# Performance work log

Hardware: AMD Instinct MI355X
Metric: run time of the kernel (lower is better)

Reference implementation:

```python
import jax, jax.numpy as jnp
import numpy as np

B, H, W, DM = 32, 32, 32, 128   # batch, height, width, d_model
DIN, N, R = 64, 16, 8           # d_inner(low_dim), d_state, dt_rank=ceil(128/16)
LN_EPS = 1e-5


def setup_inputs() -> dict:
    key = jax.random.key(0)
    ks = jax.random.split(key, 10)
    x = jax.random.normal(ks[0], (B, H, W, DM), dtype=jnp.float32)
    w_in = jax.random.normal(ks[1], (2 * DIN, DM), dtype=jnp.float32) * 0.02
    conv_w = jax.random.normal(ks[2], (DIN, 1, 3, 3), dtype=jnp.float32) * 0.1
    conv_b = jax.random.normal(ks[3], (DIN,), dtype=jnp.float32) * 0.01
    xproj_w = jax.random.normal(ks[4], (R + 2 * N, DIN), dtype=jnp.float32) * 0.05
    dtproj_w = jax.random.uniform(ks[5], (DIN, R), dtype=jnp.float32,
                                  minval=-(R ** -0.5), maxval=R ** -0.5)
    # dt bias init: inverse-softplus of dt ~ LogUniform(1e-3, 0.1)
    dt = jnp.exp(jax.random.uniform(ks[6], (DIN,)) * (np.log(0.1) - np.log(0.001)) + np.log(0.001))
    dt = jnp.clip(dt, 1e-4, None)
    dtproj_b = dt + jnp.log(-jnp.expm1(-dt))
    A_logs = jnp.log(jnp.broadcast_to(jnp.arange(1, N + 1, dtype=jnp.float32), (DIN, N)))
    Ds = jnp.ones((DIN,), dtype=jnp.float32)
    ln_g = jnp.ones((DIN,), dtype=jnp.float32)
    ln_b = jnp.zeros((DIN,), dtype=jnp.float32)
    w_out = jax.random.normal(ks[7], (DM, DIN), dtype=jnp.float32) * 0.02
    return {"x": x, "w_in": w_in, "conv_w": conv_w, "conv_b": conv_b,
            "xproj_w": xproj_w, "dtproj_w": dtproj_w, "dtproj_b": dtproj_b,
            "A_logs": A_logs, "Ds": Ds, "ln_g": ln_g, "ln_b": ln_b, "w_out": w_out}


def _silu(v):
    return v * jax.nn.sigmoid(v)


def reference(x, w_in, conv_w, conv_b, xproj_w, dtproj_w, dtproj_b,
              A_logs, Ds, ln_g, ln_b, w_out):
    b, h, w, _ = x.shape
    L = h * w
    # in_proj (no bias) and gate split
    xz = jnp.einsum('bhwc,ec->bhwe', x, w_in)           # [B,H,W,2*DIN]
    xc, z = jnp.split(xz, 2, axis=-1)
    # depthwise conv2d, SAME padding (k=3, pad=1), then SiLU
    xc = jnp.transpose(xc, (0, 3, 1, 2))                # [B,DIN,H,W]
    xc = jax.lax.conv_general_dilated(
        xc, conv_w, window_strides=(1, 1), padding=((1, 1), (1, 1)),
        feature_group_count=DIN, dimension_numbers=('NCHW', 'OIHW', 'NCHW'))
    xc = _silu(xc + conv_b[None, :, None, None])
    u = xc.reshape(b, DIN, L)                            # [B,D,L]
    # x_proj -> dt, B, C
    x_dbl = jnp.einsum('bdl,cd->bcl', u, xproj_w)        # [B,R+2N,L]
    dts, Bs, Cs = x_dbl[:, :R], x_dbl[:, R:R + N], x_dbl[:, R + N:]
    delta = jnp.einsum('brl,dr->bdl', dts, dtproj_w) + dtproj_b[None, :, None]
    delta = jax.nn.softplus(delta)                       # [B,D,L]
    A = -jnp.exp(A_logs)                                 # [D,N]
    dA = jnp.exp(delta[..., None] * A[None, :, None, :])               # [B,D,L,N]
    dBu = (delta * u)[..., None] * jnp.swapaxes(Bs, 1, 2)[:, None]     # [B,D,L,N]
    # sequential selective scan over L
    dA_s = jnp.moveaxis(dA, 2, 0)                        # [L,B,D,N]
    dBu_s = jnp.moveaxis(dBu, 2, 0)
    C_s = jnp.moveaxis(Cs, 2, 0)                         # [L,B,N]

    def step(hst, inp):
        dA_t, dBu_t, C_t = inp
        hst = dA_t * hst + dBu_t                         # [B,D,N]
        y_t = jnp.einsum('bdn,bn->bd', hst, C_t)
        return hst, y_t

    h0 = jnp.zeros((b, DIN, N), dtype=u.dtype)
    _, ys = jax.lax.scan(step, h0, (dA_s, dBu_s, C_s))   # ys: [L,B,D]
    y = jnp.moveaxis(ys, 0, 2) + Ds[None, :, None] * u   # [B,D,L]
    # back to [B,H,W,D], layernorm, gate, out_proj
    y = jnp.swapaxes(y, 1, 2).reshape(b, h, w, DIN)
    mu = jnp.mean(y, axis=-1, keepdims=True)
    var = jnp.var(y, axis=-1, keepdims=True)
    y = (y - mu) * jax.lax.rsqrt(var + LN_EPS) * ln_g + ln_b
    y = y * _silu(z)
    return jnp.einsum('bhwd,cd->bhwc', y, w_out)
```

## Files before the change

kernel.cpp:

```cpp
#include <hip/hip_runtime.h>


__global__ __launch_bounds__(256) void k1_gemm_in(
    const float* __restrict__ x, const float* __restrict__ w_in,
    float* __restrict__ xc, float* __restrict__ z)
{
    __shared__ float As[32 * 68];
    __shared__ float Ws[32 * 132];
    const int t  = threadIdx.x;
    const int p0 = blockIdx.x * 64;
    const int tx = t & 15, ty = t >> 4;

    float acc[4][8];
#pragma unroll
    for (int i = 0; i < 4; ++i)
#pragma unroll
        for (int j = 0; j < 8; ++j) acc[i][j] = 0.f;

    for (int kk = 0; kk < 128; kk += 32) {
        {
            const int m  = t >> 3;
            const int c4 = (t & 7) * 4;
            const float4 v0 = *reinterpret_cast<const float4*>(&x[(size_t)(p0 + m) * 128 + kk + c4]);
            const float4 v1 = *reinterpret_cast<const float4*>(&x[(size_t)(p0 + m + 32) * 128 + kk + c4]);
            As[(c4 + 0) * 68 + m] = v0.x; As[(c4 + 1) * 68 + m] = v0.y;
            As[(c4 + 2) * 68 + m] = v0.z; As[(c4 + 3) * 68 + m] = v0.w;
            As[(c4 + 0) * 68 + m + 32] = v1.x; As[(c4 + 1) * 68 + m + 32] = v1.y;
            As[(c4 + 2) * 68 + m + 32] = v1.z; As[(c4 + 3) * 68 + m + 32] = v1.w;
        }
        for (int i = t; i < 4096; i += 256) {
            const int c = i & 31, e = i >> 5;
            Ws[c * 132 + e] = w_in[(size_t)e * 128 + kk + c];
        }
        __syncthreads();
#pragma unroll
        for (int k = 0; k < 32; ++k) {
            const float4 a  = *reinterpret_cast<const float4*>(&As[k * 68 + (ty << 2)]);
            const float4 b0 = *reinterpret_cast<const float4*>(&Ws[k * 132 + (tx << 3)]);
            const float4 b1 = *reinterpret_cast<const float4*>(&Ws[k * 132 + (tx << 3) + 4]);
            const float am[4] = {a.x, a.y, a.z, a.w};
            const float bm[8] = {b0.x, b0.y, b0.z, b0.w, b1.x, b1.y, b1.z, b1.w};
#pragma unroll
            for (int i = 0; i < 4; ++i)
#pragma unroll
                for (int j = 0; j < 8; ++j)
                    acc[i][j] = fmaf(am[i], bm[j], acc[i][j]);
        }
        __syncthreads();
    }

    const int b  = p0 >> 10;
    const int l0 = (p0 & 1023) + (ty << 2);
    if (tx < 8) {
#pragma unroll
        for (int j = 0; j < 8; ++j) {
            const int e = (tx << 3) + j;
            *reinterpret_cast<float4*>(&xc[((size_t)b * 64 + e) * 1024 + l0]) =
                make_float4(acc[0][j], acc[1][j], acc[2][j], acc[3][j]);
        }
    } else {
        const int d0 = (tx - 8) << 3;
#pragma unroll
        for (int i = 0; i < 4; ++i) {
            const size_t p = (size_t)p0 + (ty << 2) + i;
            *reinterpret_cast<float4*>(&z[p * 64 + d0]) =
                make_float4(acc[i][0], acc[i][1], acc[i][2], acc[i][3]);
            *reinterpret_cast<float4*>(&z[p * 64 + d0 + 4]) =
                make_float4(acc[i][4], acc[i][5], acc[i][6], acc[i][7]);
        }
    }
}

__global__ __launch_bounds__(256) void k2_conv(
    const float* __restrict__ xc, const float* __restrict__ cw,
    const float* __restrict__ cb, float* __restrict__ u)
{
    __shared__ float pl[1024];
    const int bd = blockIdx.x;
    const int t  = threadIdx.x;
    const int d  = bd & 63;
    reinterpret_cast<float4*>(pl)[t] =
        reinterpret_cast<const float4*>(xc + (size_t)bd * 1024)[t];
    float w[9];
#pragma unroll
    for (int i = 0; i < 9; ++i) w[i] = cw[d * 9 + i];
    const float bias = cb[d];
    __syncthreads();
    float o[4];
#pragma unroll
    for (int i = 0; i < 4; ++i) {
        const int p  = t * 4 + i;
        const int py = p >> 5, px = p & 31;
        float s = 0.f;
#pragma unroll
        for (int ky = 0; ky < 3; ++ky) {
            const int iy = py + ky - 1;
            if (iy < 0 || iy > 31) continue;
#pragma unroll
            for (int kx = 0; kx < 3; ++kx) {
                const int ix = px + kx - 1;
                if (ix < 0 || ix > 31) continue;
                s = fmaf(pl[iy * 32 + ix], w[ky * 3 + kx], s);
            }
        }
        s += bias;
        o[i] = s / (1.f + __expf(-s));
    }
    reinterpret_cast<float4*>(u + (size_t)bd * 1024)[t] = make_float4(o[0], o[1], o[2], o[3]);
}

__global__ __launch_bounds__(256) void k3_xproj(
    const float* __restrict__ u, const float* __restrict__ xpw,
    const float* __restrict__ dtw_g, const float* __restrict__ dtb,
    float* __restrict__ delta, float* __restrict__ Bsp, float* __restrict__ Csp)
{
    __shared__ float ut[64][33];
    __shared__ float xd[40][33];
    __shared__ float xw[64 * 40];
    __shared__ float dwv[512];
    const int t   = threadIdx.x;
    const int blk = blockIdx.x;
    const int b   = blk >> 5;
    const int l0  = (blk & 31) * 32;

    for (int i = t; i < 2560; i += 256) {
        const int dd = i / 40, c = i - dd * 40;
        xw[i] = xpw[(size_t)c * 64 + dd];
    }
    for (int i = t; i < 512; i += 256) dwv[i] = dtw_g[i];

    {
        const int dd = t >> 2;
        const int lq = (t & 3) * 8;
        const float* up = u + ((size_t)b * 64 + dd) * 1024 + l0 + lq;
        const float4 v0 = *reinterpret_cast<const float4*>(up);
        const float4 v1 = *reinterpret_cast<const float4*>(up + 4);
        ut[dd][lq + 0] = v0.x; ut[dd][lq + 1] = v0.y;
        ut[dd][lq + 2] = v0.z; ut[dd][lq + 3] = v0.w;
        ut[dd][lq + 4] = v1.x; ut[dd][lq + 5] = v1.y;
        ut[dd][lq + 6] = v1.z; ut[dd][lq + 7] = v1.w;
    }
    __syncthreads();

    {
        const int pix = t & 31, cg = t >> 5;
        const int c0 = cg * 5;
        float a0 = 0.f, a1 = 0.f, a2 = 0.f, a3 = 0.f, a4 = 0.f;
#pragma unroll 8
        for (int dd = 0; dd < 64; ++dd) {
            const float uv = ut[dd][pix];
            const float* row = &xw[dd * 40 + c0];
            a0 = fmaf(uv, row[0], a0);
            a1 = fmaf(uv, row[1], a1);
            a2 = fmaf(uv, row[2], a2);
            a3 = fmaf(uv, row[3], a3);
            a4 = fmaf(uv, row[4], a4);
        }
        xd[c0 + 0][pix] = a0; xd[c0 + 1][pix] = a1; xd[c0 + 2][pix] = a2;
        xd[c0 + 3][pix] = a3; xd[c0 + 4][pix] = a4;
    }
    __syncthreads();

    {
        const int pix = t & 31, nn = t >> 5;
        float* bp = Bsp + (size_t)b * 16384 + l0 + pix;
        float* cp = Csp + (size_t)b * 16384 + l0 + pix;
        bp[(size_t)nn * 1024]       = xd[8 + nn][pix];
        bp[(size_t)(nn + 8) * 1024] = xd[16 + nn][pix];
        cp[(size_t)nn * 1024]       = xd[24 + nn][pix];
        cp[(size_t)(nn + 8) * 1024] = xd[32 + nn][pix];
    }
    {
        const int pix = t & 31;
        const int d0  = (t >> 5) * 8;
        float dts[8];
#pragma unroll
        for (int r = 0; r < 8; ++r) dts[r] = xd[r][pix];
        float* dp = delta + (size_t)b * 65536 + l0 + pix;
#pragma unroll
        for (int k = 0; k < 8; ++k) {
            const int dd = d0 + k;
            const float* r8 = &dwv[dd * 8];
            float s = dtb[dd];
            s = fmaf(dts[0], r8[0], s); s = fmaf(dts[1], r8[1], s);
            s = fmaf(dts[2], r8[2], s); s = fmaf(dts[3], r8[3], s);
            s = fmaf(dts[4], r8[4], s); s = fmaf(dts[5], r8[5], s);
            s = fmaf(dts[6], r8[6], s); s = fmaf(dts[7], r8[7], s);
            const float sp = fmaxf(s, 0.f) + log1pf(__expf(-fabsf(s)));
            dp[(size_t)dd * 1024] = sp;
        }
    }
}

__global__ __launch_bounds__(256) void k4_scan(
    const float* __restrict__ delta, const float* __restrict__ u,
    const float* __restrict__ Bsp, const float* __restrict__ Csp,
    const float* __restrict__ A_logs, const float* __restrict__ Ds,
    float* __restrict__ y)
{
    __shared__ float Ps[256][17];
    __shared__ float qs[256][17];
    __shared__ float Sp[16][17];
    __shared__ float Sq[16][17];
    const int t = threadIdx.x;
    const int pair = blockIdx.x;
    const int b = pair >> 6, d = pair & 63;

    const float4 d4 = *reinterpret_cast<const float4*>(delta + (size_t)pair * 1024 + t * 4);
    const float4 u4 = *reinterpret_cast<const float4*>(u     + (size_t)pair * 1024 + t * 4);
    const float du0 = d4.x * u4.x, du1 = d4.y * u4.y;
    const float du2 = d4.z * u4.z, du3 = d4.w * u4.w;

    const float* Bb = Bsp + (size_t)b * 16384 + t * 4;
    const float* Cb = Csp + (size_t)b * 16384 + t * 4;

    float Bc[64];
#pragma unroll
    for (int n = 0; n < 16; ++n)
        *reinterpret_cast<float4*>(&Bc[4 * n]) =
            *reinterpret_cast<const float4*>(Bb + (size_t)n * 1024);

    float A[16];
#pragma unroll
    for (int n = 0; n < 16; ++n) A[n] = -__expf(A_logs[d * 16 + n]);

#pragma unroll
    for (int n = 0; n < 16; ++n) {
        float a, P, q;
        a = __expf(d4.x * A[n]); P = a;   q = du0 * Bc[4*n+0];
        a = __expf(d4.y * A[n]); P *= a;  q = fmaf(a, q, du1 * Bc[4*n+1]);
        a = __expf(d4.z * A[n]); P *= a;  q = fmaf(a, q, du2 * Bc[4*n+2]);
        a = __expf(d4.w * A[n]); P *= a;  q = fmaf(a, q, du3 * Bc[4*n+3]);
        Ps[t][n] = P; qs[t][n] = q;
    }
    __syncthreads();

    const int n = t >> 4, g = t & 15;
    float rp[16], rq[16];
    {
        float Pseg = 1.f, qseg = 0.f;
#pragma unroll
        for (int i = 0; i < 16; ++i) {
            const int c = g * 16 + i;
            rp[i] = Ps[c][n]; rq[i] = qs[c][n];
            qseg = fmaf(rp[i], qseg, rq[i]);
            Pseg *= rp[i];
        }
        Sp[g][n] = Pseg; Sq[g][n] = qseg;
    }
    __syncthreads();
    if (t < 16) {
        float h = 0.f;
#pragma unroll
        for (int s = 0; s < 16; ++s) {
            const float Pv = Sp[s][t], qv = Sq[s][t];
            Sp[s][t] = h;
            h = fmaf(Pv, h, qv);
        }
    }
    __syncthreads();
    {
        float h = Sp[g][n];
#pragma unroll
        for (int i = 0; i < 16; ++i) {
            const int c = g * 16 + i;
            qs[c][n] = h;
            h = fmaf(rp[i], h, rq[i]);
        }
    }
    __syncthreads();

    const float Dval = Ds[d];
    float y0 = Dval * u4.x, y1 = Dval * u4.y, y2 = Dval * u4.z, y3 = Dval * u4.w;
#pragma unroll
    for (int nn = 0; nn < 16; ++nn) {
        const float4 C4 = *reinterpret_cast<const float4*>(Cb + (size_t)nn * 1024);
        float h = qs[t][nn];
        float a;
        a = __expf(d4.x * A[nn]); h = fmaf(a, h, du0 * Bc[4*nn+0]); y0 = fmaf(h, C4.x, y0);
        a = __expf(d4.y * A[nn]); h = fmaf(a, h, du1 * Bc[4*nn+1]); y1 = fmaf(h, C4.y, y1);
        a = __expf(d4.z * A[nn]); h = fmaf(a, h, du2 * Bc[4*nn+2]); y2 = fmaf(h, C4.z, y2);
        a = __expf(d4.w * A[nn]); h = fmaf(a, h, du3 * Bc[4*nn+3]); y3 = fmaf(h, C4.w, y3);
    }
    *reinterpret_cast<float4*>(y + (size_t)pair * 1024 + t * 4) =
        make_float4(y0, y1, y2, y3);
}

__global__ __launch_bounds__(256) void k5_out(
    const float* __restrict__ y, const float* __restrict__ z,
    const float* __restrict__ ln_g, const float* __restrict__ ln_b,
    const float* __restrict__ w_out, float* __restrict__ out)
{
    __shared__ float yn[64 * 68];
    __shared__ float wo[64 * 132];
    const int t  = threadIdx.x;
    const int p0 = blockIdx.x * 64;
    const int b  = p0 >> 10, l0 = p0 & 1023;

    for (int i = t; i < 8192; i += 256) {
        const int c = i >> 6, dd = i & 63;
        wo[dd * 132 + c] = w_out[i];
    }

    {
        const int d = t >> 2;
        const float* yrow = y + ((size_t)b * 64 + d) * 1024 + l0;
#pragma unroll
        for (int k = 0; k < 4; ++k) {
            const int c4 = ((t & 3) + k * 4) * 4;
            const float4 v = *reinterpret_cast<const float4*>(&yrow[c4]);
            yn[(c4 + 0) * 68 + d] = v.x;
            yn[(c4 + 1) * 68 + d] = v.y;
            yn[(c4 + 2) * 68 + d] = v.z;
            yn[(c4 + 3) * 68 + d] = v.w;
        }
    }
    __syncthreads();

    const int lane = t & 63, wv = t >> 6;
    const float g = ln_g[lane], bbv = ln_b[lane];
#pragma unroll 1
    for (int i = 0; i < 16; ++i) {
        const int pl = wv * 16 + i;
        const size_t p = (size_t)p0 + pl;
        const float v  = yn[pl * 68 + lane];
        const float zv = z[p * 64 + lane];
        float s1 = v, s2 = v * v;
#pragma unroll
        for (int m = 1; m < 64; m <<= 1) {
            s1 += __shfl_xor(s1, m);
            s2 += __shfl_xor(s2, m);
        }
        const float mu   = s1 * (1.f / 64.f);
        const float var  = s2 * (1.f / 64.f) - mu * mu;
        const float rstd = rsqrtf(var + 1e-5f);
        const float sz   = zv / (1.f + __expf(-zv));
        yn[pl * 68 + lane] = ((v - mu) * rstd * g + bbv) * sz;
    }
    __syncthreads();

    const int tx = t & 31, ty = t >> 5;
    float acc[8][4];
#pragma unroll
    for (int i = 0; i < 8; ++i)
#pragma unroll
        for (int j = 0; j < 4; ++j) acc[i][j] = 0.f;

    for (int dd = 0; dd < 64; ++dd) {
        const float4 w4 = *reinterpret_cast<const float4*>(&wo[dd * 132 + (tx << 2)]);
#pragma unroll
        for (int i = 0; i < 8; ++i) {
            const float a = yn[(ty * 8 + i) * 68 + dd];
            acc[i][0] = fmaf(a, w4.x, acc[i][0]);
            acc[i][1] = fmaf(a, w4.y, acc[i][1]);
            acc[i][2] = fmaf(a, w4.z, acc[i][2]);
            acc[i][3] = fmaf(a, w4.w, acc[i][3]);
        }
    }
#pragma unroll
    for (int i = 0; i < 8; ++i) {
        const size_t p = (size_t)p0 + ty * 8 + i;
        *reinterpret_cast<float4*>(&out[p * 128 + (tx << 2)]) =
            make_float4(acc[i][0], acc[i][1], acc[i][2], acc[i][3]);
    }
}

extern "C" void kernel_launch(void* const* d_in, const int* in_sizes, int n_in,
                              void* d_out, int out_size, void* d_ws, size_t ws_size,
                              hipStream_t stream)
{
    const float* x        = (const float*)d_in[0];
    const float* w_in     = (const float*)d_in[1];
    const float* conv_w   = (const float*)d_in[2];
    const float* conv_b   = (const float*)d_in[3];
    const float* xproj_w  = (const float*)d_in[4];
    const float* dtproj_w = (const float*)d_in[5];
    const float* dtproj_b = (const float*)d_in[6];
    const float* A_logs   = (const float*)d_in[7];
    const float* Ds       = (const float*)d_in[8];
    const float* ln_g     = (const float*)d_in[9];
    const float* ln_b     = (const float*)d_in[10];
    const float* w_out    = (const float*)d_in[11];
    float* out = (float*)d_out;
    float* ws  = (float*)d_ws;

    const size_t M  = (size_t)2097152;
    float* xc    = ws;
    float* z     = ws + M;
    float* u     = ws + 2 * M;
    float* delta = ws + 3 * M;
    float* y     = ws + 4 * M;
    float* Bsp   = ws + 5 * M;
    float* Csp   = Bsp + 524288;

    k1_gemm_in<<<512, 256, 0, stream>>>(x, w_in, xc, z);
    k2_conv<<<2048, 256, 0, stream>>>(xc, conv_w, conv_b, u);
    k3_xproj<<<1024, 256, 0, stream>>>(u, xproj_w, dtproj_w, dtproj_b, delta, Bsp, Csp);
    k4_scan<<<2048, 256, 0, stream>>>(delta, u, Bsp, Csp, A_logs, Ds, y);
    k5_out<<<512, 256, 0, stream>>>(y, z, ln_g, ln_b, w_out, out);
}
```

Before: 95.25 us.

## Fuse depthwise conv+SiLU into xproj and scan kernels, drop u buffer

```diff
diff --git a/kernel.cpp b/kernel.cpp
--- a/kernel.cpp
+++ b/kernel.cpp
@@ -71,74 +71,59 @@
     }
 }
 
-__global__ __launch_bounds__(256) void k2_conv(
+__global__ __launch_bounds__(256) void k3_xproj(
     const float* __restrict__ xc, const float* __restrict__ cw,
-    const float* __restrict__ cb, float* __restrict__ u)
-{
-    __shared__ float pl[1024];
-    const int bd = blockIdx.x;
-    const int t  = threadIdx.x;
-    const int d  = bd & 63;
-    reinterpret_cast<float4*>(pl)[t] =
-        reinterpret_cast<const float4*>(xc + (size_t)bd * 1024)[t];
-    float w[9];
-#pragma unroll
-    for (int i = 0; i < 9; ++i) w[i] = cw[d * 9 + i];
-    const float bias = cb[d];
-    __syncthreads();
-    float o[4];
-#pragma unroll
-    for (int i = 0; i < 4; ++i) {
-        const int p  = t * 4 + i;
-        const int py = p >> 5, px = p & 31;
-        float s = 0.f;
-#pragma unroll
-        for (int ky = 0; ky < 3; ++ky) {
-            const int iy = py + ky - 1;
-            if (iy < 0 || iy > 31) continue;
-#pragma unroll
-            for (int kx = 0; kx < 3; ++kx) {
-                const int ix = px + kx - 1;
-                if (ix < 0 || ix > 31) continue;
-                s = fmaf(pl[iy * 32 + ix], w[ky * 3 + kx], s);
-            }
-        }
-        s += bias;
-        o[i] = s / (1.f + __expf(-s));
-    }
-    reinterpret_cast<float4*>(u + (size_t)bd * 1024)[t] = make_float4(o[0], o[1], o[2], o[3]);
-}
-
-__global__ __launch_bounds__(256) void k3_xproj(
-    const float* __restrict__ u, const float* __restrict__ xpw,
+    const float* __restrict__ cb, const float* __restrict__ xpw,
     const float* __restrict__ dtw_g, const float* __restrict__ dtb,
     float* __restrict__ delta, float* __restrict__ Bsp, float* __restrict__ Csp)
 {
+    __shared__ float xct[64][100];
     __shared__ float ut[64][33];
-    __shared__ float xd[40][33];
-    __shared__ float xw[64 * 40];
-    __shared__ float dwv[512];
+    __shared__ float cwl[64][10];
+    __shared__ float cbl[64];
+    __shared__ float dwv[64 * 9];
+    float* xd = &xct[0][0];
+
     const int t   = threadIdx.x;
     const int blk = blockIdx.x;
     const int b   = blk >> 5;
-    const int l0  = (blk & 31) * 32;
-
-    for (int i = t; i < 2560; i += 256) {
-        const int dd = i / 40, c = i - dd * 40;
-        xw[i] = xpw[(size_t)c * 64 + dd];
-    }
-    for (int i = t; i < 512; i += 256) dwv[i] = dtw_g[i];
-
-    {
-        const int dd = t >> 2;
-        const int lq = (t & 3) * 8;
-        const float* up = u + ((size_t)b * 64 + dd) * 1024 + l0 + lq;
-        const float4 v0 = *reinterpret_cast<const float4*>(up);
-        const float4 v1 = *reinterpret_cast<const float4*>(up + 4);
-        ut[dd][lq + 0] = v0.x; ut[dd][lq + 1] = v0.y;
-        ut[dd][lq + 2] = v0.z; ut[dd][lq + 3] = v0.w;
-        ut[dd][lq + 4] = v1.x; ut[dd][lq + 5] = v1.y;
-        ut[dd][lq + 6] = v1.z; ut[dd][lq + 7] = v1.w;
+    const int s   = blk & 31;
+    const int l0  = s * 32;
+
+    for (int i = t; i < 576; i += 256) cwl[i / 9][i % 9] = cw[i];
+    if (t < 64) cbl[t] = cb[t];
+    for (int i = t; i < 512; i += 256) dwv[(i >> 3) * 9 + (i & 7)] = dtw_g[i];
+
+#pragma unroll
+    for (int k = 0; k < 6; ++k) {
+        const int j4  = t + k * 256;
+        const int dd  = j4 / 24;
+        const int rem = j4 - dd * 24;
+        const int rr  = rem >> 3, o4 = rem & 7;
+        const int row = s - 1 + rr;
+        float4 v = make_float4(0.f, 0.f, 0.f, 0.f);
+        if (row >= 0 && row < 32)
+            v = *reinterpret_cast<const float4*>(
+                xc + ((size_t)b * 64 + dd) * 1024 + row * 32 + o4 * 4);
+        *reinterpret_cast<float4*>(&xct[dd][rr * 32 + o4 * 4]) = v;
+    }
+    __syncthreads();
+
+#pragma unroll
+    for (int k = 0; k < 8; ++k) {
+        const int o  = t + k * 256;
+        const int dd = o >> 5, px = o & 31;
+        float acc = cbl[dd];
+#pragma unroll
+        for (int rr = 0; rr < 3; ++rr) {
+#pragma unroll
+            for (int kx = 0; kx < 3; ++kx) {
+                const int xx = px + kx - 1;
+                if (xx >= 0 && xx < 32)
+                    acc = fmaf(xct[dd][rr * 32 + xx], cwl[dd][rr * 3 + kx], acc);
+            }
+        }
+        ut[dd][px] = acc / (1.f + __expf(-acc));
     }
     __syncthreads();
 
@@ -149,15 +134,15 @@
 #pragma unroll 8
         for (int dd = 0; dd < 64; ++dd) {
             const float uv = ut[dd][pix];
-            const float* row = &xw[dd * 40 + c0];
-            a0 = fmaf(uv, row[0], a0);
-            a1 = fmaf(uv, row[1], a1);
-            a2 = fmaf(uv, row[2], a2);
-            a3 = fmaf(uv, row[3], a3);
-            a4 = fmaf(uv, row[4], a4);
-        }
-        xd[c0 + 0][pix] = a0; xd[c0 + 1][pix] = a1; xd[c0 + 2][pix] = a2;
-        xd[c0 + 3][pix] = a3; xd[c0 + 4][pix] = a4;
+            a0 = fmaf(uv, xpw[(size_t)(c0 + 0) * 64 + dd], a0);
+            a1 = fmaf(uv, xpw[(size_t)(c0 + 1) * 64 + dd], a1);
+            a2 = fmaf(uv, xpw[(size_t)(c0 + 2) * 64 + dd], a2);
+            a3 = fmaf(uv, xpw[(size_t)(c0 + 3) * 64 + dd], a3);
+            a4 = fmaf(uv, xpw[(size_t)(c0 + 4) * 64 + dd], a4);
+        }
+        xd[(c0 + 0) * 33 + pix] = a0; xd[(c0 + 1) * 33 + pix] = a1;
+        xd[(c0 + 2) * 33 + pix] = a2; xd[(c0 + 3) * 33 + pix] = a3;
+        xd[(c0 + 4) * 33 + pix] = a4;
     }
     __syncthreads();
 
@@ -165,35 +150,33 @@
         const int pix = t & 31, nn = t >> 5;
         float* bp = Bsp + (size_t)b * 16384 + l0 + pix;
         float* cp = Csp + (size_t)b * 16384 + l0 + pix;
-        bp[(size_t)nn * 1024]       = xd[8 + nn][pix];
-        bp[(size_t)(nn + 8) * 1024] = xd[16 + nn][pix];
-        cp[(size_t)nn * 1024]       = xd[24 + nn][pix];
-        cp[(size_t)(nn + 8) * 1024] = xd[32 + nn][pix];
+        bp[(size_t)nn * 1024]       = xd[(8 + nn) * 33 + pix];
+        bp[(size_t)(nn + 8) * 1024] = xd[(16 + nn) * 33 + pix];
+        cp[(size_t)nn * 1024]       = xd[(24 + nn) * 33 + pix];
+        cp[(size_t)(nn + 8) * 1024] = xd[(32 + nn) * 33 + pix];
     }
     {
         const int pix = t & 31;
         const int d0  = (t >> 5) * 8;
         float dts[8];
 #pragma unroll
-        for (int r = 0; r < 8; ++r) dts[r] = xd[r][pix];
+        for (int r = 0; r < 8; ++r) dts[r] = xd[r * 33 + pix];
         float* dp = delta + (size_t)b * 65536 + l0 + pix;
 #pragma unroll
         for (int k = 0; k < 8; ++k) {
             const int dd = d0 + k;
-            const float* r8 = &dwv[dd * 8];
-            float s = dtb[dd];
-            s = fmaf(dts[0], r8[0], s); s = fmaf(dts[1], r8[1], s);
-            s = fmaf(dts[2], r8[2], s); s = fmaf(dts[3], r8[3], s);
-            s = fmaf(dts[4], r8[4], s); s = fmaf(dts[5], r8[5], s);
-            s = fmaf(dts[6], r8[6], s); s = fmaf(dts[7], r8[7], s);
-            const float sp = fmaxf(s, 0.f) + log1pf(__expf(-fabsf(s)));
-            dp[(size_t)dd * 1024] = sp;
+            const float* r8 = &dwv[dd * 9];
+            float sv = dtb[dd];
+#pragma unroll
+            for (int r = 0; r < 8; ++r) sv = fmaf(dts[r], r8[r], sv);
+            dp[(size_t)dd * 1024] = fmaxf(sv, 0.f) + log1pf(__expf(-fabsf(sv)));
         }
     }
 }
 
 __global__ __launch_bounds__(256) void k4_scan(
-    const float* __restrict__ delta, const float* __restrict__ u,
+    const float* __restrict__ xc, const float* __restrict__ cw,
+    const float* __restrict__ cb, const float* __restrict__ delta,
     const float* __restrict__ Bsp, const float* __restrict__ Csp,
     const float* __restrict__ A_logs, const float* __restrict__ Ds,
     float* __restrict__ y)
@@ -202,12 +185,46 @@
     __shared__ float qs[256][17];
     __shared__ float Sp[16][17];
     __shared__ float Sq[16][17];
+    float* pl = &Ps[0][0];
+
     const int t = threadIdx.x;
     const int pair = blockIdx.x;
     const int b = pair >> 6, d = pair & 63;
 
+    *reinterpret_cast<float4*>(&pl[t * 4]) =
+        *reinterpret_cast<const float4*>(xc + (size_t)pair * 1024 + t * 4);
+    float w9[9];
+#pragma unroll
+    for (int i = 0; i < 9; ++i) w9[i] = cw[d * 9 + i];
+    const float cbias = cb[d];
     const float4 d4 = *reinterpret_cast<const float4*>(delta + (size_t)pair * 1024 + t * 4);
-    const float4 u4 = *reinterpret_cast<const float4*>(u     + (size_t)pair * 1024 + t * 4);
+    __syncthreads();
+
+    float4 u4;
+    {
+        float uo[4];
+#pragma unroll
+        for (int i = 0; i < 4; ++i) {
+            const int p  = t * 4 + i;
+            const int py = p >> 5, px = p & 31;
+            float s = cbias;
+#pragma unroll
+            for (int ky = 0; ky < 3; ++ky) {
+                const int iy = py + ky - 1;
+                if (iy < 0 || iy > 31) continue;
+#pragma unroll
+                for (int kx = 0; kx < 3; ++kx) {
+                    const int ix = px + kx - 1;
+                    if (ix < 0 || ix > 31) continue;
+                    s = fmaf(pl[iy * 32 + ix], w9[ky * 3 + kx], s);
+                }
+            }
+            uo[i] = s / (1.f + __expf(-s));
+        }
+        u4 = make_float4(uo[0], uo[1], uo[2], uo[3]);
+    }
+    __syncthreads();
+
     const float du0 = d4.x * u4.x, du1 = d4.y * u4.y;
     const float du2 = d4.z * u4.z, du3 = d4.w * u4.w;
 
@@ -387,15 +404,15 @@
     const size_t M  = (size_t)2097152;
     float* xc    = ws;
     float* z     = ws + M;
-    float* u     = ws + 2 * M;
     float* delta = ws + 3 * M;
     float* y     = ws + 4 * M;
     float* Bsp   = ws + 5 * M;
     float* Csp   = Bsp + 524288;
 
     k1_gemm_in<<<512, 256, 0, stream>>>(x, w_in, xc, z);
-    k2_conv<<<2048, 256, 0, stream>>>(xc, conv_w, conv_b, u);
-    k3_xproj<<<1024, 256, 0, stream>>>(u, xproj_w, dtproj_w, dtproj_b, delta, Bsp, Csp);
-    k4_scan<<<2048, 256, 0, stream>>>(delta, u, Bsp, Csp, A_logs, Ds, y);
+    k3_xproj<<<1024, 256, 0, stream>>>(xc, conv_w, conv_b, xproj_w,
+                                       dtproj_w, dtproj_b, delta, Bsp, Csp);
+    k4_scan<<<2048, 256, 0, stream>>>(xc, conv_w, conv_b, delta, Bsp, Csp,
+                                      A_logs, Ds, y);
     k5_out<<<512, 256, 0, stream>>>(y, z, ln_g, ln_b, w_out, out);
 }
```

Result: slower. 100.1 us (+5.1%).
